# Performance work log

Hardware: AMD Instinct MI355X
Metric: run time of the kernel (lower is better)

Reference implementation:

```python
import jax, jax.numpy as jnp
import numpy as np

N_HEADS, D_MODEL, D_HEAD, N_CTX = 16, 1024, 64, 2048
IGNORE = -100000.0


def setup_inputs() -> dict:
    key = jax.random.key(0)
    ks = jax.random.split(key, 8)
    B, S = 2, 2048
    return {
        "query_input": jax.random.normal(ks[0], (B, S, D_MODEL), jnp.float32),
        "key_input": jax.random.normal(ks[1], (B, S, D_MODEL), jnp.float32),
        "value_input": jax.random.normal(ks[2], (B, S, D_MODEL), jnp.float32),
        "additive_attention_mask": jnp.zeros((B, 1, 1, S), jnp.float32),
        "W_Q": jax.random.normal(ks[3], (N_HEADS, D_MODEL, D_HEAD), jnp.float32) * 0.02,
        "W_K": jax.random.normal(ks[4], (N_HEADS, D_MODEL, D_HEAD), jnp.float32) * 0.02,
        "W_V": jax.random.normal(ks[5], (N_HEADS, D_MODEL, D_HEAD), jnp.float32) * 0.02,
        "W_O": jax.random.normal(ks[6], (N_HEADS, D_HEAD, D_MODEL), jnp.float32) * 0.02,
        "b_Q": jnp.zeros((N_HEADS, D_HEAD), jnp.float32),
        "b_K": jnp.zeros((N_HEADS, D_HEAD), jnp.float32),
        "b_V": jnp.zeros((N_HEADS, D_HEAD), jnp.float32),
        "b_O": jnp.zeros((D_MODEL,), jnp.float32),
    }


def reference(query_input, key_input, value_input, additive_attention_mask,
              W_Q, W_K, W_V, W_O, b_Q, b_K, b_V, b_O):
    attn_scale = jnp.float32(np.sqrt(D_HEAD))
    # [batch, pos, head, d_head]
    q = jnp.einsum('bpm,hmd->bphd', query_input, W_Q) + b_Q
    k = jnp.einsum('bpm,hmd->bphd', key_input, W_K) + b_K
    v = jnp.einsum('bpm,hmd->bphd', value_input, W_V) + b_V
    # [batch, head, query_pos, key_pos]
    attn_scores = jnp.einsum('bqhd,bkhd->bhqk', q, k) / attn_scale
    S_q, S_k = attn_scores.shape[-2], attn_scores.shape[-1]
    causal = jnp.tril(jnp.ones((N_CTX, N_CTX), bool))[:S_q, :S_k]
    attn_scores = jnp.where(causal, attn_scores, jnp.float32(IGNORE))
    attn_scores = attn_scores + additive_attention_mask
    pattern = jax.nn.softmax(attn_scores, axis=-1)
    z = jnp.einsum('bkhd,bhqk->bqhd', v, pattern)
    out = jnp.einsum('bqhd,hdm->bqm', z, W_O) + b_O
    return out
```

## Files before the change

### kernel.cpp

```cpp
#include <hip/hip_runtime.h>
#include <hip/hip_bf16.h>

typedef __attribute__((ext_vector_type(8))) short s8;
typedef __attribute__((ext_vector_type(4))) short s4;
typedef __attribute__((ext_vector_type(4))) float f4;
typedef unsigned short u16;

__device__ __forceinline__ u16 f2bf(float f){
  union { float f; unsigned int i; } v; v.f = f;
  unsigned int x = v.i;
  return (u16)((x + 0x7fffu + ((x >> 16) & 1u)) >> 16);
}
__device__ __forceinline__ unsigned pk2bf(float a, float b){
  __hip_bfloat162 h = __float22bfloat162_rn(float2{a, b});
  union { __hip_bfloat162 h; unsigned u; } c; c.h = h; return c.u;
}
__device__ __forceinline__ s8 ld8(const u16* p){
  return *reinterpret_cast<const s8*>(p);
}
__device__ __forceinline__ void async16(const u16* g, u16* l){
  __builtin_amdgcn_global_load_lds(
      (const __attribute__((address_space(1))) unsigned int*)(g),
      (__attribute__((address_space(3))) unsigned int*)(l),
      16, 0, 0);
}

#define MFMA16(a, b, c) __builtin_amdgcn_mfma_f32_16x16x32_bf16((a), (b), (c), 0, 0, 0)

__global__ __launch_bounds__(256) void cvt_x(
    const float* __restrict__ x0, const float* __restrict__ x1,
    const float* __restrict__ x2, u16* __restrict__ dst)
{
  const int m = blockIdx.y;
  const float* src = m == 0 ? x0 : (m == 1 ? x1 : x2);
  u16* d = dst + (size_t)m * 4194304;
  const size_t i = ((size_t)blockIdx.x * 256 + threadIdx.x) * 8;
  const float4 a = *reinterpret_cast<const float4*>(src + i);
  const float4 b = *reinterpret_cast<const float4*>(src + i + 4);
  s8 o;
  o[0] = (short)f2bf(a.x); o[1] = (short)f2bf(a.y);
  o[2] = (short)f2bf(a.z); o[3] = (short)f2bf(a.w);
  o[4] = (short)f2bf(b.x); o[5] = (short)f2bf(b.y);
  o[6] = (short)f2bf(b.z); o[7] = (short)f2bf(b.w);
  *reinterpret_cast<s8*>(d + i) = o;
}

__global__ __launch_bounds__(256) void transpose_qkv(
    const float* __restrict__ wq, const float* __restrict__ wk, const float* __restrict__ wv,
    u16* __restrict__ tq, u16* __restrict__ tk, u16* __restrict__ tv)
{
  __shared__ __align__(16) u16 tile[64 * 65];
  const int mat = blockIdx.z, h = blockIdx.y, kt = blockIdx.x;
  const float* W = mat == 0 ? wq : (mat == 1 ? wk : wv);
  u16*         O = mat == 0 ? tq : (mat == 1 ? tk : tv);
  const float* src = W + (size_t)h * 65536;
  u16*         dst = O + (size_t)h * 65536;
  const int t = threadIdx.x;
  const int k0 = kt * 64;
  #pragma unroll
  for (int i = 0; i < 16; ++i) {
    int idx = i * 256 + t;
    int kr = idx >> 6, d = idx & 63;
    tile[kr * 65 + d] = f2bf(src[(size_t)(k0 + kr) * 64 + d]);
  }
  __syncthreads();
  #pragma unroll
  for (int i = 0; i < 16; ++i) {
    int idx = i * 256 + t;
    int d = idx >> 6, kr = idx & 63;
    dst[(size_t)d * 1024 + k0 + kr] = tile[kr * 65 + d];
  }
}

__global__ __launch_bounds__(256) void transpose_wo(
    const float* __restrict__ src, u16* __restrict__ dst)
{
  __shared__ __align__(16) u16 tile[64 * 65];
  const int r0 = blockIdx.y * 64, c0 = blockIdx.x * 64;
  const int t = threadIdx.x;
  #pragma unroll
  for (int i = 0; i < 16; ++i) {
    int idx = i * 256 + t;
    int rr = idx >> 6, cc = idx & 63;
    tile[rr * 65 + cc] = f2bf(src[(size_t)(r0 + rr) * 1024 + c0 + cc]);
  }
  __syncthreads();
  #pragma unroll
  for (int i = 0; i < 16; ++i) {
    int idx = i * 256 + t;
    int cc = idx >> 6, rr = idx & 63;
    dst[(size_t)(c0 + cc) * 1024 + r0 + rr] = tile[rr * 65 + cc];
  }
}

__global__ __launch_bounds__(256) void qkv_proj(
    const u16* __restrict__ Xb,
    const u16* __restrict__ wtq, const u16* __restrict__ wtk, const u16* __restrict__ wtv,
    const float* __restrict__ bq, const float* __restrict__ bk, const float* __restrict__ bv,
    u16* __restrict__ Qo, u16* __restrict__ Ko, u16* __restrict__ Vto)
{
  constexpr int BST = 40;
  __shared__ __align__(16) u16 Bl[64 * BST];
  const int proj = blockIdx.y >> 4;
  const int h    = blockIdx.y & 15;
  const u16* X    = Xb + (size_t)proj * 4194304;
  const u16* Wt   = proj == 0 ? wtq : (proj == 1 ? wtk : wtv);
  const float* bi = proj == 0 ? bq  : (proj == 1 ? bk  : bv);
  const int t = threadIdx.x;
  const int wave = t >> 6, lane = t & 63, lm = lane & 15, quad = lane >> 4;
  const int row0 = blockIdx.x * 64 + wave * 16;
  const u16* Wb = Wt + (size_t)(h * 64) * 1024;
  f4 acc[4] = {f4{0,0,0,0}, f4{0,0,0,0}, f4{0,0,0,0}, f4{0,0,0,0}};
  const int sr = t >> 2, scol = (t & 3) * 8;
  for (int k0 = 0; k0 < 1024; k0 += 32) {
    *reinterpret_cast<s8*>(&Bl[sr * BST + scol]) = ld8(Wb + (size_t)sr * 1024 + k0 + scol);
    __syncthreads();
    s8 a = ld8(X + (size_t)(row0 + lm) * 1024 + k0 + quad * 8);
    #pragma unroll
    for (int nt = 0; nt < 4; ++nt) {
      s8 b = *reinterpret_cast<const s8*>(&Bl[(nt * 16 + lm) * BST + quad * 8]);
      acc[nt] = MFMA16(a, b, acc[nt]);
    }
    __syncthreads();
  }
  const int batch = row0 >> 11;
  const int pos0  = (row0 & 2047) + quad * 4;
  #pragma unroll
  for (int nt = 0; nt < 4; ++nt) {
    const int d = nt * 16 + lm;
    const float bb = bi[h * 64 + d];
    if (proj == 2) {
      s4 pk;
      #pragma unroll
      for (int r = 0; r < 4; ++r) pk[r] = (short)f2bf(acc[nt][r] + bb);
      *reinterpret_cast<s4*>(Vto + ((size_t)((batch * 16 + h) * 64 + d)) * 2048 + pos0) = pk;
    } else {
      u16* O = proj == 0 ? Qo : Ko;
      const size_t base = ((size_t)(batch * 16 + h)) * 2048;
      #pragma unroll
      for (int r = 0; r < 4; ++r)
        O[(base + pos0 + r) * 64 + d] = f2bf(acc[nt][r] + bb);
    }
  }
}

__global__ __launch_bounds__(256) void attn(
    const u16* __restrict__ Q, const u16* __restrict__ K, const u16* __restrict__ Vt,
    const float* __restrict__ amask, u16* __restrict__ Z)
{
  constexpr int PST = 68;
  __shared__ __align__(16) u16 KL[2][4096];
  __shared__ __align__(16) u16 VL[2][4096];
  __shared__ __align__(16) u16 Pl[4][16 * PST];
  const int wg  = blockIdx.x;
  const int xcd = wg & 7, idx = wg >> 3;
  const int qi  = idx >> 2, bhl = idx & 3;
  const int qc  = 31 - qi;
  const int bh  = xcd * 4 + bhl;
  const int b   = bh >> 4, h = bh & 15;
  const int t = threadIdx.x, wave = t >> 6, lane = t & 63;
  const int lm = lane & 15, quad = lane >> 4;
  const u16* Qb = Q + (size_t)bh * 131072;
  const u16* Kb = K + (size_t)bh * 131072;
  const u16* Vb = Vt + (size_t)bh * 131072;
  const float* mk = amask + b * 2048;
  u16* Pw = Pl[wave];
  const int qw0 = qc * 64 + wave * 16;
  const int q = qw0 + lm;
  const s8 bQ0 = ld8(Qb + (size_t)q * 64 + quad * 8);
  const s8 bQ1 = ld8(Qb + (size_t)q * 64 + 32 + quad * 8);

  const int lr = lane >> 3;
  const int sw = (lane & 7) ^ lr;
  const int c0 = 2 * wave;
  const u16* pK0 = Kb + (c0 * 8 + lr) * 64 + sw * 8;
  const u16* pK1 = pK0 + 512;
  const u16* pV0 = Vb + (size_t)(c0 * 8 + lr) * 2048 + sw * 8;
  const u16* pV1 = pV0 + 8 * 2048;
  const int ldso = c0 * 512;

  const int fb0 = lm * 64 + ((quad ^ (lm & 7)) * 8);
  const int fb1 = lm * 64 + (((4 + quad) ^ (lm & 7)) * 8);

  f4 o[4] = {f4{0,0,0,0}, f4{0,0,0,0}, f4{0,0,0,0}, f4{0,0,0,0}};
  float psum = 0.f;
  const int nT = qc + 1;
  const float SC = 0.125f * 1.44269504f;

  async16(pK0, &KL[0][ldso]);       async16(pK1, &KL[0][ldso + 512]);
  async16(pV0, &VL[0][ldso]);       async16(pV1, &VL[0][ldso + 512]);
  pK0 += 4096; pK1 += 4096; pV0 += 64; pV1 += 64;

  for (int kt = 0; kt < nT; ++kt) {
    __syncthreads();
    if (kt + 1 < nT) {
      const int nb = (kt + 1) & 1;
      async16(pK0, &KL[nb][ldso]);   async16(pK1, &KL[nb][ldso + 512]);
      async16(pV0, &VL[nb][ldso]);   async16(pV1, &VL[nb][ldso + 512]);
      pK0 += 4096; pK1 += 4096; pV0 += 64; pV1 += 64;
    }
    const u16* Kc = KL[kt & 1];
    const u16* Vc = VL[kt & 1];
    const int k0 = kt * 64;
    f4 sc[4] = {f4{0,0,0,0}, f4{0,0,0,0}, f4{0,0,0,0}, f4{0,0,0,0}};
    #pragma unroll
    for (int nt = 0; nt < 4; ++nt) {
      sc[nt] = MFMA16(ld8(Kc + fb0 + nt * 1024), bQ0, sc[nt]);
      sc[nt] = MFMA16(ld8(Kc + fb1 + nt * 1024), bQ1, sc[nt]);
    }
    const bool masked = (kt == nT - 1);
    #pragma unroll
    for (int nt = 0; nt < 4; ++nt) {
      const int key0 = k0 + nt * 16 + quad * 4;
      const float4 mv = *reinterpret_cast<const float4*>(mk + key0);
      float p[4];
      if (masked) {
        #pragma unroll
        for (int r = 0; r < 4; ++r) {
          float s = (key0 + r <= q)
                    ? sc[nt][r] * SC + (&mv.x)[r] * 1.44269504f
                    : -__builtin_inff();
          p[r] = exp2f(s);
        }
      } else {
        #pragma unroll
        for (int r = 0; r < 4; ++r)
          p[r] = exp2f(sc[nt][r] * SC + (&mv.x)[r] * 1.44269504f);
      }
      psum += (p[0] + p[1]) + (p[2] + p[3]);
      *reinterpret_cast<uint2*>(&Pw[lm * PST + nt * 16 + quad * 4]) =
          uint2{pk2bf(p[0], p[1]), pk2bf(p[2], p[3])};
    }
    __asm__ volatile("" ::: "memory");
    #pragma unroll
    for (int kb = 0; kb < 2; ++kb) {
      s8 bP = *reinterpret_cast<const s8*>(&Pw[lm * PST + kb * 32 + quad * 8]);
      const int fb = kb ? fb1 : fb0;
      #pragma unroll
      for (int nt = 0; nt < 4; ++nt)
        o[nt] = MFMA16(ld8(Vc + fb + nt * 1024), bP, o[nt]);
    }
    __asm__ volatile("" ::: "memory");
  }

  psum += __shfl_xor(psum, 16, 64);
  psum += __shfl_xor(psum, 32, 64);
  const float inv = 1.0f / psum;
  u16* zr = Z + (size_t)(b * 2048 + q) * 1024 + h * 64;
  #pragma unroll
  for (int nt = 0; nt < 4; ++nt) {
    s4 pk;
    #pragma unroll
    for (int r = 0; r < 4; ++r) pk[r] = (short)f2bf(o[nt][r] * inv);
    *reinterpret_cast<s4*>(zr + nt * 16 + quad * 4) = pk;
  }
}

__global__ __launch_bounds__(256) void out_proj(
    const u16* __restrict__ Zi, const u16* __restrict__ Wto,
    const float* __restrict__ bO, float* __restrict__ Out)
{
  constexpr int BST = 40;
  __shared__ __align__(16) u16 Bl[64 * BST];
  const int t = threadIdx.x;
  const int wave = t >> 6, lane = t & 63, lm = lane & 15, quad = lane >> 4;
  const int row0 = blockIdx.x * 64 + wave * 16;
  const int nb = blockIdx.y * 64;
  const u16* Wb = Wto + (size_t)nb * 1024;
  f4 acc[4] = {f4{0,0,0,0}, f4{0,0,0,0}, f4{0,0,0,0}, f4{0,0,0,0}};
  const int sr = t >> 2, scol = (t & 3) * 8;
  for (int k0 = 0; k0 < 1024; k0 += 32) {
    *reinterpret_cast<s8*>(&Bl[sr * BST + scol]) = ld8(Wb + (size_t)sr * 1024 + k0 + scol);
    __syncthreads();
    s8 a = ld8(Zi + (size_t)(row0 + lm) * 1024 + k0 + quad * 8);
    #pragma unroll
    for (int nt = 0; nt < 4; ++nt) {
      s8 b = *reinterpret_cast<const s8*>(&Bl[(nt * 16 + lm) * BST + quad * 8]);
      acc[nt] = MFMA16(a, b, acc[nt]);
    }
    __syncthreads();
  }
  #pragma unroll
  for (int nt = 0; nt < 4; ++nt) {
    const int n = nb + nt * 16 + lm;
    const float bb = bO[n];
    #pragma unroll
    for (int r = 0; r < 4; ++r) {
      const int row = row0 + quad * 4 + r;
      Out[(size_t)row * 1024 + n] = acc[nt][r] + bb;
    }
  }
}

extern "C" void kernel_launch(void* const* d_in, const int* in_sizes, int n_in,
                              void* d_out, int out_size, void* d_ws, size_t ws_size,
                              hipStream_t stream)
{
  const float* xq = (const float*)d_in[0];
  const float* xk = (const float*)d_in[1];
  const float* xv = (const float*)d_in[2];
  const float* am = (const float*)d_in[3];
  const float* wq = (const float*)d_in[4];
  const float* wk = (const float*)d_in[5];
  const float* wv = (const float*)d_in[6];
  const float* wo = (const float*)d_in[7];
  const float* bq = (const float*)d_in[8];
  const float* bk = (const float*)d_in[9];
  const float* bv = (const float*)d_in[10];
  const float* bo = (const float*)d_in[11];
  u16* ws = (u16*)d_ws;
  const size_t M1 = 1u << 20;
  u16* Wtq = ws;
  u16* Wtk = ws + 1 * M1;
  u16* Wtv = ws + 2 * M1;
  u16* Wto = ws + 3 * M1;
  u16* Xb  = ws + 4 * M1;
  u16* Qw  = ws + 16 * M1;
  u16* Kw  = ws + 20 * M1;
  u16* Vtw = ws + 24 * M1;
  u16* Zw  = ws + 28 * M1;

  cvt_x<<<dim3(2048, 3), 256, 0, stream>>>(xq, xk, xv, Xb);
  transpose_qkv<<<dim3(16, 16, 3), 256, 0, stream>>>(wq, wk, wv, Wtq, Wtk, Wtv);
  transpose_wo<<<dim3(16, 16), 256, 0, stream>>>(wo, Wto);
  qkv_proj<<<dim3(64, 48), 256, 0, stream>>>(Xb, Wtq, Wtk, Wtv,
                                             bq, bk, bv, Qw, Kw, Vtw);
  attn<<<dim3(1024), 256, 0, stream>>>(Qw, Kw, Vtw, am, Zw);
  out_proj<<<dim3(64, 16), 256, 0, stream>>>(Zw, Wto, bo, (float*)d_out);
}
```

Baseline: 267.5 us.

## Merge prep kernels and retile projection GEMMs to 128x128 with async LDS loads

Merges the three conversion and transpose kernels into a single prep launch. Both projection GEMMs are replaced with 128x128 tiles per block, where each wave computes 64x64 using async global-to-LDS loads of A and B into XOR-swizzled shared memory; this raises operand reuse and cuts per-k-step global traffic. The attention kernel's P buffer switches from padded rows to an XOR swizzle and gets a launch-bounds occupancy hint. In exchange, the GEMMs launch fewer blocks (768 and 256) and the per-block K loop has no double buffering.

```diff
diff --git a/kernel.cpp b/kernel.cpp
--- a/kernel.cpp
+++ b/kernel.cpp
@@ -27,131 +27,184 @@
 
 #define MFMA16(a, b, c) __builtin_amdgcn_mfma_f32_16x16x32_bf16((a), (b), (c), 0, 0, 0)
 
-__global__ __launch_bounds__(256) void cvt_x(
-    const float* __restrict__ x0, const float* __restrict__ x1,
-    const float* __restrict__ x2, u16* __restrict__ dst)
-{
-  const int m = blockIdx.y;
-  const float* src = m == 0 ? x0 : (m == 1 ? x1 : x2);
-  u16* d = dst + (size_t)m * 4194304;
-  const size_t i = ((size_t)blockIdx.x * 256 + threadIdx.x) * 8;
-  const float4 a = *reinterpret_cast<const float4*>(src + i);
-  const float4 b = *reinterpret_cast<const float4*>(src + i + 4);
-  s8 o;
-  o[0] = (short)f2bf(a.x); o[1] = (short)f2bf(a.y);
-  o[2] = (short)f2bf(a.z); o[3] = (short)f2bf(a.w);
-  o[4] = (short)f2bf(b.x); o[5] = (short)f2bf(b.y);
-  o[6] = (short)f2bf(b.z); o[7] = (short)f2bf(b.w);
-  *reinterpret_cast<s8*>(d + i) = o;
-}
-
-__global__ __launch_bounds__(256) void transpose_qkv(
+__global__ __launch_bounds__(256) void prep(
     const float* __restrict__ wq, const float* __restrict__ wk, const float* __restrict__ wv,
-    u16* __restrict__ tq, u16* __restrict__ tk, u16* __restrict__ tv)
+    const float* __restrict__ wo,
+    const float* __restrict__ x0, const float* __restrict__ x1, const float* __restrict__ x2,
+    u16* __restrict__ Wt, u16* __restrict__ Wto, u16* __restrict__ Xb)
 {
   __shared__ __align__(16) u16 tile[64 * 65];
-  const int mat = blockIdx.z, h = blockIdx.y, kt = blockIdx.x;
-  const float* W = mat == 0 ? wq : (mat == 1 ? wk : wv);
-  u16*         O = mat == 0 ? tq : (mat == 1 ? tk : tv);
-  const float* src = W + (size_t)h * 65536;
-  u16*         dst = O + (size_t)h * 65536;
-  const int t = threadIdx.x;
-  const int k0 = kt * 64;
-  #pragma unroll
-  for (int i = 0; i < 16; ++i) {
-    int idx = i * 256 + t;
-    int kr = idx >> 6, d = idx & 63;
-    tile[kr * 65 + d] = f2bf(src[(size_t)(k0 + kr) * 64 + d]);
-  }
-  __syncthreads();
-  #pragma unroll
-  for (int i = 0; i < 16; ++i) {
-    int idx = i * 256 + t;
-    int d = idx >> 6, kr = idx & 63;
-    dst[(size_t)d * 1024 + k0 + kr] = tile[kr * 65 + d];
-  }
-}
-
-__global__ __launch_bounds__(256) void transpose_wo(
-    const float* __restrict__ src, u16* __restrict__ dst)
-{
-  __shared__ __align__(16) u16 tile[64 * 65];
-  const int r0 = blockIdx.y * 64, c0 = blockIdx.x * 64;
-  const int t = threadIdx.x;
-  #pragma unroll
-  for (int i = 0; i < 16; ++i) {
-    int idx = i * 256 + t;
-    int rr = idx >> 6, cc = idx & 63;
-    tile[rr * 65 + cc] = f2bf(src[(size_t)(r0 + rr) * 1024 + c0 + cc]);
-  }
-  __syncthreads();
-  #pragma unroll
-  for (int i = 0; i < 16; ++i) {
-    int idx = i * 256 + t;
-    int cc = idx >> 6, rr = idx & 63;
-    dst[(size_t)(c0 + cc) * 1024 + r0 + rr] = tile[rr * 65 + cc];
-  }
-}
-
-__global__ __launch_bounds__(256) void qkv_proj(
-    const u16* __restrict__ Xb,
-    const u16* __restrict__ wtq, const u16* __restrict__ wtk, const u16* __restrict__ wtv,
+  const int id = blockIdx.x, t = threadIdx.x;
+  if (id < 768) {
+    const int mat = id >> 8, rem = id & 255, h = rem >> 4, kt = rem & 15;
+    const float* W = mat == 0 ? wq : (mat == 1 ? wk : wv);
+    const float* src = W + (size_t)h * 65536;
+    u16* dst = Wt + (size_t)mat * 1048576 + (size_t)h * 65536;
+    const int k0 = kt * 64;
+    #pragma unroll
+    for (int i = 0; i < 16; ++i) {
+      int idx = i * 256 + t, kr = idx >> 6, d = idx & 63;
+      tile[kr * 65 + d] = f2bf(src[(size_t)(k0 + kr) * 64 + d]);
+    }
+    __syncthreads();
+    #pragma unroll
+    for (int i = 0; i < 16; ++i) {
+      int idx = i * 256 + t, d = idx >> 6, kr = idx & 63;
+      dst[(size_t)d * 1024 + k0 + kr] = tile[kr * 65 + d];
+    }
+  } else if (id < 1024) {
+    const int j = id - 768, r0 = (j >> 4) * 64, c0 = (j & 15) * 64;
+    #pragma unroll
+    for (int i = 0; i < 16; ++i) {
+      int idx = i * 256 + t, rr = idx >> 6, cc = idx & 63;
+      tile[rr * 65 + cc] = f2bf(wo[(size_t)(r0 + rr) * 1024 + c0 + cc]);
+    }
+    __syncthreads();
+    #pragma unroll
+    for (int i = 0; i < 16; ++i) {
+      int idx = i * 256 + t, cc = idx >> 6, rr = idx & 63;
+      Wto[(size_t)(c0 + cc) * 1024 + r0 + rr] = tile[rr * 65 + cc];
+    }
+  } else {
+    const int j = id - 1024, m = j >> 11, xi = j & 2047;
+    const float* src = m == 0 ? x0 : (m == 1 ? x1 : x2);
+    u16* d = Xb + (size_t)m * 4194304;
+    const size_t i = ((size_t)xi * 256 + t) * 8;
+    const float4 a = *reinterpret_cast<const float4*>(src + i);
+    const float4 b = *reinterpret_cast<const float4*>(src + i + 4);
+    s8 o;
+    o[0] = (short)f2bf(a.x); o[1] = (short)f2bf(a.y);
+    o[2] = (short)f2bf(a.z); o[3] = (short)f2bf(a.w);
+    o[4] = (short)f2bf(b.x); o[5] = (short)f2bf(b.y);
+    o[6] = (short)f2bf(b.z); o[7] = (short)f2bf(b.w);
+    *reinterpret_cast<s8*>(d + i) = o;
+  }
+}
+
+#define GEMM_CORE(Aptr, Bptr)                                                  \
+  f4 acc[4][4] = {};                                                           \
+  {                                                                            \
+    const int sr8 = lane >> 3;                                                 \
+    const int sblk = (lane & 7) ^ sr8;                                         \
+    const u16* pa = (Aptr) + (size_t)(wave * 32 + sr8) * 1024 + sblk * 8;      \
+    const u16* pb = (Bptr) + (size_t)(wave * 32 + sr8) * 1024 + sblk * 8;      \
+    u16* la = &AL[wave * 2048];                                                \
+    u16* lb = &BL[wave * 2048];                                                \
+    const int e = lm & 7;                                                      \
+    for (int k0 = 0; k0 < 1024; k0 += 64) {                                    \
+      _Pragma("unroll")                                                        \
+      for (int j = 0; j < 4; ++j) {                                            \
+        async16(pa + (size_t)j * 8192 + k0, la + j * 512);                     \
+        async16(pb + (size_t)j * 8192 + k0, lb + j * 512);                     \
+      }                                                                        \
+      __syncthreads();                                                         \
+      _Pragma("unroll")                                                        \
+      for (int kb = 0; kb < 2; ++kb) {                                         \
+        s8 af[4], bf[4];                                                       \
+        _Pragma("unroll")                                                      \
+        for (int i = 0; i < 4; ++i) {                                          \
+          af[i] = ld8(&AL[(wm + i * 16 + lm) * 64 + (((kb * 4 + quad) ^ e) * 8)]); \
+          bf[i] = ld8(&BL[(wn + i * 16 + lm) * 64 + (((kb * 4 + quad) ^ e) * 8)]); \
+        }                                                                      \
+        _Pragma("unroll")                                                      \
+        for (int mt = 0; mt < 4; ++mt)                                         \
+          _Pragma("unroll")                                                    \
+          for (int nt = 0; nt < 4; ++nt)                                       \
+            acc[mt][nt] = MFMA16(af[mt], bf[nt], acc[mt][nt]);                 \
+      }                                                                        \
+      __syncthreads();                                                         \
+    }                                                                          \
+  }
+
+__global__ __launch_bounds__(256, 2) void qkv_gemm(
+    const u16* __restrict__ Xb, const u16* __restrict__ Wt,
     const float* __restrict__ bq, const float* __restrict__ bk, const float* __restrict__ bv,
     u16* __restrict__ Qo, u16* __restrict__ Ko, u16* __restrict__ Vto)
 {
-  constexpr int BST = 40;
-  __shared__ __align__(16) u16 Bl[64 * BST];
-  const int proj = blockIdx.y >> 4;
-  const int h    = blockIdx.y & 15;
-  const u16* X    = Xb + (size_t)proj * 4194304;
-  const u16* Wt   = proj == 0 ? wtq : (proj == 1 ? wtk : wtv);
-  const float* bi = proj == 0 ? bq  : (proj == 1 ? bk  : bv);
-  const int t = threadIdx.x;
-  const int wave = t >> 6, lane = t & 63, lm = lane & 15, quad = lane >> 4;
-  const int row0 = blockIdx.x * 64 + wave * 16;
-  const u16* Wb = Wt + (size_t)(h * 64) * 1024;
-  f4 acc[4] = {f4{0,0,0,0}, f4{0,0,0,0}, f4{0,0,0,0}, f4{0,0,0,0}};
-  const int sr = t >> 2, scol = (t & 3) * 8;
-  for (int k0 = 0; k0 < 1024; k0 += 32) {
-    *reinterpret_cast<s8*>(&Bl[sr * BST + scol]) = ld8(Wb + (size_t)sr * 1024 + k0 + scol);
-    __syncthreads();
-    s8 a = ld8(X + (size_t)(row0 + lm) * 1024 + k0 + quad * 8);
+  __shared__ __align__(16) u16 AL[128 * 64];
+  __shared__ __align__(16) u16 BL[128 * 64];
+  const int tM = blockIdx.x, tN = blockIdx.y;
+  const int proj = (tN * 128) >> 10;
+  const u16* A = Xb + (size_t)proj * 4194304 + (size_t)tM * 131072;
+  const u16* B = Wt + (size_t)tN * 131072;
+  const int t = threadIdx.x, wave = t >> 6, lane = t & 63;
+  const int lm = lane & 15, quad = lane >> 4;
+  const int wm = (wave & 1) * 64, wn = (wave >> 1) * 64;
+  GEMM_CORE(A, B)
+  const int mb = tM * 128 + wm;
+  const int nb = tN * 128 + wn;
+  if (proj < 2) {
+    u16* O = proj == 0 ? Qo : Ko;
+    const float* bi = proj == 0 ? bq : bk;
     #pragma unroll
     for (int nt = 0; nt < 4; ++nt) {
-      s8 b = *reinterpret_cast<const s8*>(&Bl[(nt * 16 + lm) * BST + quad * 8]);
-      acc[nt] = MFMA16(a, b, acc[nt]);
-    }
-    __syncthreads();
-  }
-  const int batch = row0 >> 11;
-  const int pos0  = (row0 & 2047) + quad * 4;
+      const int nl = (nb + nt * 16 + lm) & 1023;
+      const int h = nl >> 6, d = nl & 63;
+      const float bb = bi[nl];
+      #pragma unroll
+      for (int mt = 0; mt < 4; ++mt) {
+        const int m = mb + mt * 16 + quad * 4;
+        const size_t base = ((size_t)((m >> 11) * 16 + h) * 2048 + (m & 2047)) * 64 + d;
+        #pragma unroll
+        for (int r = 0; r < 4; ++r)
+          O[base + (size_t)r * 64] = f2bf(acc[mt][nt][r] + bb);
+      }
+    }
+  } else {
+    #pragma unroll
+    for (int nt = 0; nt < 4; ++nt) {
+      const int nl = (nb + nt * 16 + lm) & 1023;
+      const int h = nl >> 6, d = nl & 63;
+      const float bb = bv[nl];
+      #pragma unroll
+      for (int mt = 0; mt < 4; ++mt) {
+        const int m = mb + mt * 16 + quad * 4;
+        s4 pk;
+        #pragma unroll
+        for (int r = 0; r < 4; ++r) pk[r] = (short)f2bf(acc[mt][nt][r] + bb);
+        *reinterpret_cast<s4*>(
+            Vto + ((size_t)((m >> 11) * 16 + h) * 64 + d) * 2048 + (m & 2047)) = pk;
+      }
+    }
+  }
+}
+
+__global__ __launch_bounds__(256, 2) void out_gemm(
+    const u16* __restrict__ Zi, const u16* __restrict__ Wto,
+    const float* __restrict__ bO, float* __restrict__ Out)
+{
+  __shared__ __align__(16) u16 AL[128 * 64];
+  __shared__ __align__(16) u16 BL[128 * 64];
+  const int tM = blockIdx.x, tN = blockIdx.y;
+  const u16* A = Zi + (size_t)tM * 131072;
+  const u16* B = Wto + (size_t)tN * 131072;
+  const int t = threadIdx.x, wave = t >> 6, lane = t & 63;
+  const int lm = lane & 15, quad = lane >> 4;
+  const int wm = (wave & 1) * 64, wn = (wave >> 1) * 64;
+  GEMM_CORE(A, B)
+  const int mb = tM * 128 + wm;
+  const int nb = tN * 128 + wn;
   #pragma unroll
   for (int nt = 0; nt < 4; ++nt) {
-    const int d = nt * 16 + lm;
-    const float bb = bi[h * 64 + d];
-    if (proj == 2) {
-      s4 pk;
-      #pragma unroll
-      for (int r = 0; r < 4; ++r) pk[r] = (short)f2bf(acc[nt][r] + bb);
-      *reinterpret_cast<s4*>(Vto + ((size_t)((batch * 16 + h) * 64 + d)) * 2048 + pos0) = pk;
-    } else {
-      u16* O = proj == 0 ? Qo : Ko;
-      const size_t base = ((size_t)(batch * 16 + h)) * 2048;
+    const int n = nb + nt * 16 + lm;
+    const float bb = bO[n];
+    #pragma unroll
+    for (int mt = 0; mt < 4; ++mt) {
+      const int m = mb + mt * 16 + quad * 4;
       #pragma unroll
       for (int r = 0; r < 4; ++r)
-        O[(base + pos0 + r) * 64 + d] = f2bf(acc[nt][r] + bb);
-    }
-  }
-}
-
-__global__ __launch_bounds__(256) void attn(
+        Out[(size_t)(m + r) * 1024 + n] = acc[mt][nt][r] + bb;
+    }
+  }
+}
+
+__global__ __launch_bounds__(256, 4) void attn(
     const u16* __restrict__ Q, const u16* __restrict__ K, const u16* __restrict__ Vt,
     const float* __restrict__ amask, u16* __restrict__ Z)
 {
-  constexpr int PST = 68;
   __shared__ __align__(16) u16 KL[2][4096];
   __shared__ __align__(16) u16 VL[2][4096];
-  __shared__ __align__(16) u16 Pl[4][16 * PST];
+  __shared__ __align__(16) u16 Pl[4][1024];
   const int wg  = blockIdx.x;
   const int xcd = wg & 7, idx = wg >> 3;
   const int qi  = idx >> 2, bhl = idx & 3;
@@ -179,8 +232,9 @@
   const u16* pV1 = pV0 + 8 * 2048;
   const int ldso = c0 * 512;
 
-  const int fb0 = lm * 64 + ((quad ^ (lm & 7)) * 8);
-  const int fb1 = lm * 64 + (((4 + quad) ^ (lm & 7)) * 8);
+  const int e = lm & 7;
+  const int fb0 = lm * 64 + ((quad ^ e) * 8);
+  const int fb1 = lm * 64 + (((4 + quad) ^ e) * 8);
 
   f4 o[4] = {f4{0,0,0,0}, f4{0,0,0,0}, f4{0,0,0,0}, f4{0,0,0,0}};
   float psum = 0.f;
@@ -194,9 +248,9 @@
   for (int kt = 0; kt < nT; ++kt) {
     __syncthreads();
     if (kt + 1 < nT) {
-      const int nb = (kt + 1) & 1;
-      async16(pK0, &KL[nb][ldso]);   async16(pK1, &KL[nb][ldso + 512]);
-      async16(pV0, &VL[nb][ldso]);   async16(pV1, &VL[nb][ldso + 512]);
+      const int nb2 = (kt + 1) & 1;
+      async16(pK0, &KL[nb2][ldso]);  async16(pK1, &KL[nb2][ldso + 512]);
+      async16(pV0, &VL[nb2][ldso]);  async16(pV1, &VL[nb2][ldso + 512]);
       pK0 += 4096; pK1 += 4096; pV0 += 64; pV1 += 64;
     }
     const u16* Kc = KL[kt & 1];
@@ -228,13 +282,15 @@
           p[r] = exp2f(sc[nt][r] * SC + (&mv.x)[r] * 1.44269504f);
       }
       psum += (p[0] + p[1]) + (p[2] + p[3]);
-      *reinterpret_cast<uint2*>(&Pw[lm * PST + nt * 16 + quad * 4]) =
+      const int wblk = (nt * 2 + (quad >> 1)) ^ e;
+      *reinterpret_cast<uint2*>(&Pw[lm * 64 + wblk * 8 + (quad & 1) * 4]) =
           uint2{pk2bf(p[0], p[1]), pk2bf(p[2], p[3])};
     }
     __asm__ volatile("" ::: "memory");
     #pragma unroll
     for (int kb = 0; kb < 2; ++kb) {
-      s8 bP = *reinterpret_cast<const s8*>(&Pw[lm * PST + kb * 32 + quad * 8]);
+      const int rblk = (kb * 4 + quad) ^ e;
+      s8 bP = ld8(&Pw[lm * 64 + rblk * 8]);
       const int fb = kb ? fb1 : fb0;
       #pragma unroll
       for (int nt = 0; nt < 4; ++nt)
@@ -253,42 +309,6 @@
     #pragma unroll
     for (int r = 0; r < 4; ++r) pk[r] = (short)f2bf(o[nt][r] * inv);
     *reinterpret_cast<s4*>(zr + nt * 16 + quad * 4) = pk;
-  }
-}
-
-__global__ __launch_bounds__(256) void out_proj(
-    const u16* __restrict__ Zi, const u16* __restrict__ Wto,
-    const float* __restrict__ bO, float* __restrict__ Out)
-{
-  constexpr int BST = 40;
-  __shared__ __align__(16) u16 Bl[64 * BST];
-  const int t = threadIdx.x;
-  const int wave = t >> 6, lane = t & 63, lm = lane & 15, quad = lane >> 4;
-  const int row0 = blockIdx.x * 64 + wave * 16;
-  const int nb = blockIdx.y * 64;
-  const u16* Wb = Wto + (size_t)nb * 1024;
-  f4 acc[4] = {f4{0,0,0,0}, f4{0,0,0,0}, f4{0,0,0,0}, f4{0,0,0,0}};
-  const int sr = t >> 2, scol = (t & 3) * 8;
-  for (int k0 = 0; k0 < 1024; k0 += 32) {
-    *reinterpret_cast<s8*>(&Bl[sr * BST + scol]) = ld8(Wb + (size_t)sr * 1024 + k0 + scol);
-    __syncthreads();
-    s8 a = ld8(Zi + (size_t)(row0 + lm) * 1024 + k0 + quad * 8);
-    #pragma unroll
-    for (int nt = 0; nt < 4; ++nt) {
-      s8 b = *reinterpret_cast<const s8*>(&Bl[(nt * 16 + lm) * BST + quad * 8]);
-      acc[nt] = MFMA16(a, b, acc[nt]);
-    }
-    __syncthreads();
-  }
-  #pragma unroll
-  for (int nt = 0; nt < 4; ++nt) {
-    const int n = nb + nt * 16 + lm;
-    const float bb = bO[n];
-    #pragma unroll
-    for (int r = 0; r < 4; ++r) {
-      const int row = row0 + quad * 4 + r;
-      Out[(size_t)row * 1024 + n] = acc[nt][r] + bb;
-    }
   }
 }
 
@@ -310,9 +330,7 @@
   const float* bo = (const float*)d_in[11];
   u16* ws = (u16*)d_ws;
   const size_t M1 = 1u << 20;
-  u16* Wtq = ws;
-  u16* Wtk = ws + 1 * M1;
-  u16* Wtv = ws + 2 * M1;
+  u16* Wt  = ws;
   u16* Wto = ws + 3 * M1;
   u16* Xb  = ws + 4 * M1;
   u16* Qw  = ws + 16 * M1;
@@ -320,11 +338,8 @@
   u16* Vtw = ws + 24 * M1;
   u16* Zw  = ws + 28 * M1;
 
-  cvt_x<<<dim3(2048, 3), 256, 0, stream>>>(xq, xk, xv, Xb);
-  transpose_qkv<<<dim3(16, 16, 3), 256, 0, stream>>>(wq, wk, wv, Wtq, Wtk, Wtv);
-  transpose_wo<<<dim3(16, 16), 256, 0, stream>>>(wo, Wto);
-  qkv_proj<<<dim3(64, 48), 256, 0, stream>>>(Xb, Wtq, Wtk, Wtv,
-                                             bq, bk, bv, Qw, Kw, Vtw);
+  prep<<<dim3(7168), 256, 0, stream>>>(wq, wk, wv, wo, xq, xk, xv, Wt, Wto, Xb);
+  qkv_gemm<<<dim3(32, 24), 256, 0, stream>>>(Xb, Wt, bq, bk, bv, Qw, Kw, Vtw);
   attn<<<dim3(1024), 256, 0, stream>>>(Qw, Kw, Vtw, am, Zw);
-  out_proj<<<dim3(64, 16), 256, 0, stream>>>(Zw, Wto, bo, (float*)d_out);
-}
+  out_gemm<<<dim3(32, 8), 256, 0, stream>>>(Zw, Wto, bo, (float*)d_out);
+}
```

Result: faster. 222.1 us (-16.9%).
